# Kernel tuning notes

Measured on AMD Instinct MI355X. Metric: run time of the kernel, lower is better.

The kernel has to match this reference:

```python
import jax, jax.numpy as jnp
import numpy as np

K = 10  # neighbor_num from init_kwargs


def setup_inputs() -> dict:
    key = jax.random.key(0)
    k1, k2 = jax.random.split(key)
    xyz = jax.random.normal(k1, (8, 16384, 3), dtype=jnp.float32)
    sample_xyz = jax.random.normal(k2, (8, 1024, 3), dtype=jnp.float32)
    temp = jnp.ones((), dtype=jnp.float32)  # init_temp = 1.0
    return {"xyz": xyz, "sample_xyz": sample_xyz, "temp": temp}


def reference(xyz, sample_xyz, temp):
    # Pairwise squared distances [B, S, N] via ||a-b||^2 = ||a||^2 + ||b||^2 - 2 a.b
    q2 = jnp.sum(sample_xyz * sample_xyz, axis=-1)            # [B, S]
    p2 = jnp.sum(xyz * xyz, axis=-1)                          # [B, N]
    cross = jnp.einsum('bsd,bnd->bsn', sample_xyz, xyz)       # [B, S, N]
    d2 = q2[:, :, None] + p2[:, None, :] - 2.0 * cross
    d2 = jnp.maximum(d2, 0.0)
    # K nearest neighbors (smallest squared distance)
    neg_top, idx = jax.lax.top_k(-d2, K)                      # [B, S, K]
    squared_dist = -neg_top
    # Gather neighbor coordinates: [B, S, K, 3]
    neighbor_xyz = jax.vmap(lambda pts, ids: pts[ids])(xyz, idx)
    # Softmax weights over the K neighbors
    weight = jax.nn.softmax(-squared_dist / (temp * temp), axis=-1)  # [B, S, K]
    proj_xyz = jnp.sum(neighbor_xyz * weight[..., None], axis=-2)    # [B, S, 3]
    return (proj_xyz, temp)
```

## Files before the change

kernel.cpp:

```cpp
#include <hip/hip_runtime.h>
#include <math.h>

#define NPTS 16384
#define NSMP 8192
#define KNN 10
#define QPB 8
#define WAVES 4
#define SLICE 4096
#define GPW 32
#define CAP 64
#define LCAP 128

typedef float v2f __attribute__((ext_vector_type(2)));
typedef unsigned long long u64;

__device__ __forceinline__ unsigned mapf(float f) {
    unsigned u = __float_as_uint(f);
    return (u & 0x80000000u) ? ~u : (u | 0x80000000u);
}
__device__ __forceinline__ float unmapf(unsigned k) {
    unsigned u = (k & 0x80000000u) ? (k ^ 0x80000000u) : ~k;
    return __uint_as_float(u);
}
__device__ __forceinline__ float uniform_f(float x) {
    return __uint_as_float(__builtin_amdgcn_readfirstlane(__float_as_uint(x)));
}

__global__ __launch_bounds__(256) void pack_kernel(const float* __restrict__ xyz,
                                                   float4* __restrict__ pk,
                                                   float4* __restrict__ pk2) {
    const int t = blockIdx.x * 256 + threadIdx.x;
    const int b = t >> 13;
    const int r = t & 8191;
    const int g = r >> 6;
    const int l = r & 63;
    const float* pA = xyz + ((size_t)b * NPTS + (size_t)g * 128 + l) * 3;
    const float* pB = pA + 64 * 3;
    const float xA = pA[0], yA = pA[1], zA = pA[2];
    const float xB = pB[0], yB = pB[1], zB = pB[2];
    const float wA = fmaf(xA, xA, fmaf(yA, yA, zA * zA));
    const float wB = fmaf(xB, xB, fmaf(yB, yB, zB * zB));
    float4* dst = pk + ((size_t)(b * 128 + g) * 128);
    dst[l]      = make_float4(xA, xB, yA, yB);
    dst[l + 64] = make_float4(zA, zB, wA, wB);
    float4* dst2 = pk2 + (size_t)b * NPTS + (size_t)g * 128;
    dst2[l]      = make_float4(xA, yA, zA, wA);
    dst2[l + 64] = make_float4(xB, yB, zB, wB);
}

__global__ __launch_bounds__(256) void knn_kernel(
    const float4* __restrict__ pk,
    const float4* __restrict__ pk2,
    const float* __restrict__ sxyz,
    const float* __restrict__ temp,
    float* __restrict__ out)
{
    __shared__ float minBuf[QPB][512];
    __shared__ int   cnt[QPB];
    __shared__ int   list[WAVES][LCAP];
    __shared__ u64   candK[QPB][CAP];
    __shared__ u64   sort10[QPB][KNN];

    const int lane  = threadIdx.x & 63;
    const int w     = threadIdx.x >> 6;
    const int qbase = blockIdx.x * QPB;
    const int b     = qbase >> 10;

    if (threadIdx.x < QPB) cnt[threadIdx.x] = 0;

    float ax[QPB], ay[QPB], az[QPB];
    #pragma unroll
    for (int q = 0; q < QPB; ++q) {
        const float* s = sxyz + (size_t)(qbase + q) * 3;
        ax[q] = uniform_f(-2.f * s[0]);
        ay[q] = uniform_f(-2.f * s[1]);
        az[q] = uniform_f(-2.f * s[2]);
    }

    const float4* pw = pk + ((size_t)(b * 128 + w * 32)) * 128 + lane;

    v2f mn[QPB];
    #pragma unroll
    for (int q = 0; q < QPB; ++q) { mn[q].x = INFINITY; mn[q].y = INFINITY; }

    #pragma unroll 1
    for (int j = 0; j < GPW; j += 2) {
        const float4 a0 = pw[(size_t)(j + 0) * 128], a1 = pw[(size_t)(j + 0) * 128 + 64];
        const float4 b0 = pw[(size_t)(j + 1) * 128], b1 = pw[(size_t)(j + 1) * 128 + 64];
        {
            const v2f X = {a0.x, a0.y}, Y = {a0.z, a0.w}, Z = {a1.x, a1.y}, W = {a1.z, a1.w};
            #pragma unroll
            for (int q = 0; q < QPB; ++q) {
                const v2f d = X * ax[q] + (Y * ay[q] + (Z * az[q] + W));
                mn[q] = __builtin_elementwise_min(mn[q], d);
            }
        }
        {
            const v2f X = {b0.x, b0.y}, Y = {b0.z, b0.w}, Z = {b1.x, b1.y}, W = {b1.z, b1.w};
            #pragma unroll
            for (int q = 0; q < QPB; ++q) {
                const v2f d = X * ax[q] + (Y * ay[q] + (Z * az[q] + W));
                mn[q] = __builtin_elementwise_min(mn[q], d);
            }
        }
    }
    #pragma unroll
    for (int q = 0; q < QPB; ++q) {
        minBuf[q][w * 128 + lane]      = mn[q].x;
        minBuf[q][w * 128 + 64 + lane] = mn[q].y;
    }
    __syncthreads();

    const float4* p2 = pk2 + (size_t)b * NPTS;
    const float t = temp[0];
    const float invt2 = 1.0f / (t * t);

    #pragma unroll 1
    for (int qi = 0; qi < 2; ++qi) {
        const int rq  = w + qi * WAVES;
        const int gid = qbase + rq;
        const float* sq = sxyz + (size_t)gid * 3;
        const float bx = -2.f * sq[0], by = -2.f * sq[1], bz = -2.f * sq[2];

        float mh[8];
        #pragma unroll
        for (int s8 = 0; s8 < 8; ++s8)
            mh[s8] = minBuf[rq][(s8 >> 1) * 128 + (s8 & 1) * 64 + lane];

        float vm = mh[0];
        #pragma unroll
        for (int s8 = 1; s8 < 8; ++s8) vm = fminf(vm, mh[s8]);
        const unsigned um = mapf(vm);
        unsigned lo = 0u, hi = 0xFFFFFFFFu;
        #pragma unroll 1
        for (int it = 0; it < 16; ++it) {
            const unsigned mid = lo + ((hi - lo) >> 1);
            const int c = __popcll(__ballot(um <= mid));
            if (c >= KNN) hi = mid; else lo = mid + 1;
        }
        const float tau = unmapf(hi);

        int nf = 0;
        #pragma unroll
        for (int s8 = 0; s8 < 8; ++s8) {
            const bool flg = (mh[s8] <= tau);
            const u64 m = __ballot(flg);
            const int pos = nf + __popcll(m & ((1ull << lane) - 1ull));
            if (flg && pos < LCAP) list[w][pos] = (s8 >> 1) * 128 + (s8 & 1) * 64 + lane;
            nf += __popcll(m);
        }
        if (nf > LCAP) nf = LCAP;

        const int total = nf * 32;
        for (int i = lane; i < total; i += 64) {
            const int s   = list[w][i >> 5];
            const int idx = ((s >> 7) << 12) + ((i & 31) << 7) + (s & 127);
            const float4 pt = p2[idx];
            const float d = fmaf(pt.x, bx, fmaf(pt.y, by, fmaf(pt.z, bz, pt.w)));
            if (d <= tau) {
                const int sl = atomicAdd(&cnt[rq], 1);
                if (sl < CAP) candK[rq][sl] = ((u64)mapf(d) << 32) | (unsigned)idx;
            }
        }

        const int c = min(cnt[rq], CAP);
        const u64 k0 = (lane < c) ? candK[rq][lane] : ~0ull;
        int r0 = 0;
        for (int jj = 0; jj < c; ++jj) {
            const u64 kj = candK[rq][jj];
            r0 += (kj < k0) ? 1 : 0;
        }
        if (lane < c && r0 < KNN) sort10[rq][r0] = k0;
        const u64 sel = (lane < KNN) ? sort10[rq][lane] : ~0ull;

        const float q2 = fmaf(sq[0], sq[0], fmaf(sq[1], sq[1], sq[2] * sq[2]));
        const float dp = unmapf((unsigned)(sel >> 32));
        const float d2v = fmaxf(dp + q2, 0.f);
        const float dmin = __shfl(d2v, 0);
        float wgt = 0.f, px = 0.f, py = 0.f, pz = 0.f;
        if (lane < KNN) {
            wgt = __expf((dmin - d2v) * invt2);
            const int idx = (int)(unsigned)(sel & 0xFFFFFFFFull);
            const float4 pp = p2[idx];
            px = pp.x; py = pp.y; pz = pp.z;
        }
        float sw = wgt, sx = wgt * px, sy = wgt * py, sz = wgt * pz;
        #pragma unroll
        for (int off = 8; off >= 1; off >>= 1) {
            sw += __shfl_xor(sw, off);
            sx += __shfl_xor(sx, off);
            sy += __shfl_xor(sy, off);
            sz += __shfl_xor(sz, off);
        }
        if (lane == 0) {
            const float inv = 1.0f / sw;
            out[(size_t)gid * 3 + 0] = sx * inv;
            out[(size_t)gid * 3 + 1] = sy * inv;
            out[(size_t)gid * 3 + 2] = sz * inv;
            if (gid == 0) out[NSMP * 3] = t;
        }
    }
}

extern "C" void kernel_launch(void* const* d_in, const int* in_sizes, int n_in,
                              void* d_out, int out_size, void* d_ws, size_t ws_size,
                              hipStream_t stream) {
    const float* xyz  = (const float*)d_in[0];
    const float* sxyz = (const float*)d_in[1];
    const float* temp = (const float*)d_in[2];
    float* out = (float*)d_out;

    float4* pk  = (float4*)d_ws;
    float4* pk2 = (float4*)((char*)d_ws + (size_t)131072*16);

    hipLaunchKernelGGL(pack_kernel, dim3(256), dim3(256), 0, stream, xyz, pk, pk2);
    hipLaunchKernelGGL(knn_kernel, dim3(NSMP / QPB), dim3(256), 0, stream,
                       pk, pk2, sxyz, temp, out);
}
```

Before: 40.08 us.

## Split KNN point scan into two halves per query block and merge top-k

Each query group now runs as two blocks, each scanning half of the point cloud and writing its local top-10 candidates to workspace. A new merge kernel ranks the 20 candidates per query, selects the 10 nearest and computes the softmax-weighted projection. This doubles the block count for better occupancy and shortens the per-block serial scan, at the cost of an extra kernel launch, a workspace round trip, and recomputing the threshold search and filtering in each half.

```diff
diff --git a/kernel.cpp b/kernel.cpp
--- a/kernel.cpp
+++ b/kernel.cpp
@@ -6,10 +6,10 @@
 #define KNN 10
 #define QPB 8
 #define WAVES 4
-#define SLICE 4096
-#define GPW 32
-#define CAP 64
-#define LCAP 128
+#define HALF 8192
+#define GPW 16
+#define CAP 48
+#define LCAP 96
 
 typedef float v2f __attribute__((ext_vector_type(2)));
 typedef unsigned long long u64;
@@ -52,8 +52,7 @@
     const float4* __restrict__ pk,
     const float4* __restrict__ pk2,
     const float* __restrict__ sxyz,
-    const float* __restrict__ temp,
-    float* __restrict__ out)
+    u64* __restrict__ ws2)
 {
     __shared__ float minBuf[QPB][512];
     __shared__ int   cnt[QPB];
@@ -63,7 +62,9 @@
 
     const int lane  = threadIdx.x & 63;
     const int w     = threadIdx.x >> 6;
-    const int qbase = blockIdx.x * QPB;
+    const int h     = blockIdx.x & 1;
+    const int qg    = blockIdx.x >> 1;
+    const int qbase = qg * QPB;
     const int b     = qbase >> 10;
 
     if (threadIdx.x < QPB) cnt[threadIdx.x] = 0;
@@ -77,7 +78,7 @@
         az[q] = uniform_f(-2.f * s[2]);
     }
 
-    const float4* pw = pk + ((size_t)(b * 128 + w * 32)) * 128 + lane;
+    const float4* pw = pk + ((size_t)(b * 128 + h * 64 + w * 16)) * 128 + lane;
 
     v2f mn[QPB];
     #pragma unroll
@@ -112,8 +113,6 @@
     __syncthreads();
 
     const float4* p2 = pk2 + (size_t)b * NPTS;
-    const float t = temp[0];
-    const float invt2 = 1.0f / (t * t);
 
     #pragma unroll 1
     for (int qi = 0; qi < 2; ++qi) {
@@ -151,10 +150,11 @@
         }
         if (nf > LCAP) nf = LCAP;
 
-        const int total = nf * 32;
+        const int total = nf * 16;
         for (int i = lane; i < total; i += 64) {
-            const int s   = list[w][i >> 5];
-            const int idx = ((s >> 7) << 12) + ((i & 31) << 7) + (s & 127);
+            const int sid = list[w][i >> 4];
+            const int p   = i & 15;
+            const int idx = ((h * 64 + ((sid >> 7) << 4) + p) << 7) + (sid & 127);
             const float4 pt = p2[idx];
             const float d = fmaf(pt.x, bx, fmaf(pt.y, by, fmaf(pt.z, bz, pt.w)));
             if (d <= tau) {
@@ -171,34 +171,60 @@
             r0 += (kj < k0) ? 1 : 0;
         }
         if (lane < c && r0 < KNN) sort10[rq][r0] = k0;
-        const u64 sel = (lane < KNN) ? sort10[rq][lane] : ~0ull;
-
-        const float q2 = fmaf(sq[0], sq[0], fmaf(sq[1], sq[1], sq[2] * sq[2]));
-        const float dp = unmapf((unsigned)(sel >> 32));
-        const float d2v = fmaxf(dp + q2, 0.f);
-        const float dmin = __shfl(d2v, 0);
-        float wgt = 0.f, px = 0.f, py = 0.f, pz = 0.f;
-        if (lane < KNN) {
-            wgt = __expf((dmin - d2v) * invt2);
-            const int idx = (int)(unsigned)(sel & 0xFFFFFFFFull);
-            const float4 pp = p2[idx];
-            px = pp.x; py = pp.y; pz = pp.z;
-        }
-        float sw = wgt, sx = wgt * px, sy = wgt * py, sz = wgt * pz;
-        #pragma unroll
-        for (int off = 8; off >= 1; off >>= 1) {
-            sw += __shfl_xor(sw, off);
-            sx += __shfl_xor(sx, off);
-            sy += __shfl_xor(sy, off);
-            sz += __shfl_xor(sz, off);
-        }
-        if (lane == 0) {
-            const float inv = 1.0f / sw;
-            out[(size_t)gid * 3 + 0] = sx * inv;
-            out[(size_t)gid * 3 + 1] = sy * inv;
-            out[(size_t)gid * 3 + 2] = sz * inv;
-            if (gid == 0) out[NSMP * 3] = t;
-        }
+        if (lane < KNN) ws2[(size_t)gid * (2 * KNN) + h * KNN + lane] = sort10[rq][lane];
+    }
+}
+
+__global__ __launch_bounds__(256) void merge_kernel(
+    const u64* __restrict__ ws2,
+    const float* __restrict__ xyz,
+    const float* __restrict__ sxyz,
+    const float* __restrict__ temp,
+    float* __restrict__ out)
+{
+    const int lane = threadIdx.x & 63;
+    const int gid  = blockIdx.x * 4 + (threadIdx.x >> 6);
+    const int b    = gid >> 10;
+
+    const u64 k = (lane < 2 * KNN) ? ws2[(size_t)gid * (2 * KNN) + lane] : ~0ull;
+    int r = 0;
+    #pragma unroll
+    for (int jj = 0; jj < 2 * KNN; ++jj) {
+        const u64 kj = __shfl(k, jj);
+        r += (kj < k) ? 1 : 0;
+    }
+    const unsigned long long mm = __ballot(r == 0 && lane < 2 * KNN);
+    const u64 kmin = __shfl(k, (int)__builtin_ctzll(mm));
+
+    const float* s = sxyz + (size_t)gid * 3;
+    const float q2 = fmaf(s[0], s[0], fmaf(s[1], s[1], s[2] * s[2]));
+    const float t = temp[0];
+    const float invt2 = 1.0f / (t * t);
+    const float dmin = fmaxf(unmapf((unsigned)(kmin >> 32)) + q2, 0.f);
+
+    const bool sel = (lane < 2 * KNN) && (r < KNN);
+    float wgt = 0.f, px = 0.f, py = 0.f, pz = 0.f;
+    if (sel) {
+        const float d2v = fmaxf(unmapf((unsigned)(k >> 32)) + q2, 0.f);
+        wgt = __expf((dmin - d2v) * invt2);
+        const int idx = (int)(unsigned)(k & 0xFFFFFFFFull);
+        const float* pp = xyz + ((size_t)b * NPTS + idx) * 3;
+        px = pp[0]; py = pp[1]; pz = pp[2];
+    }
+    float sw = wgt, sx = wgt * px, sy = wgt * py, sz = wgt * pz;
+    #pragma unroll
+    for (int off = 16; off >= 1; off >>= 1) {
+        sw += __shfl_xor(sw, off);
+        sx += __shfl_xor(sx, off);
+        sy += __shfl_xor(sy, off);
+        sz += __shfl_xor(sz, off);
+    }
+    if (lane == 0) {
+        const float inv = 1.0f / sw;
+        out[(size_t)gid * 3 + 0] = sx * inv;
+        out[(size_t)gid * 3 + 1] = sy * inv;
+        out[(size_t)gid * 3 + 2] = sz * inv;
+        if (gid == 0) out[NSMP * 3] = t;
     }
 }
 
@@ -211,9 +237,12 @@
     float* out = (float*)d_out;
 
     float4* pk  = (float4*)d_ws;
-    float4* pk2 = (float4*)((char*)d_ws + (size_t)131072*16);
+    float4* pk2 = (float4*)((char*)d_ws + (size_t)131072 * 16);
+    u64*    ws2 = (u64*)((char*)d_ws + (size_t)262144 * 16);
 
     hipLaunchKernelGGL(pack_kernel, dim3(256), dim3(256), 0, stream, xyz, pk, pk2);
-    hipLaunchKernelGGL(knn_kernel, dim3(NSMP / QPB), dim3(256), 0, stream,
-                       pk, pk2, sxyz, temp, out);
-}
+    hipLaunchKernelGGL(knn_kernel, dim3(NSMP / QPB * 2), dim3(256), 0, stream,
+                       pk, pk2, sxyz, ws2);
+    hipLaunchKernelGGL(merge_kernel, dim3(NSMP / 4), dim3(256), 0, stream,
+                       ws2, xyz, sxyz, temp, out);
+}
```

New measurement: 44.53 us. +11.1%, slower.
